# Kernel optimization log

Hardware: AMD Instinct MI355X
Metric: run time of the kernel (lower is better)

Reference implementation:

```python
import jax, jax.numpy as jnp
import numpy as np

IMG_H, IMG_W = 800.0, 1280.0
STRIDE = 16
SCALE = 1.0 / STRIDE
P, S = 14, 1              # pooler resolution, sampling ratio
NUM_CLASSES = 80
BBOX_W = (10.0, 10.0, 5.0, 5.0)
SCORE_TH, NMS_TH, MAX_DET, IOU_TH = 0.05, 0.5, 100, 0.5
SCALE_CLAMP = float(np.log(1000.0 / 16.0))


def _make_boxes(key, n_img, n_box):
    k1, k2, k3, k4 = jax.random.split(key, 4)
    x1 = jax.random.uniform(k1, (n_img, n_box)) * (IMG_W - 64.0)
    y1 = jax.random.uniform(k2, (n_img, n_box)) * (IMG_H - 64.0)
    w = jax.random.uniform(k3, (n_img, n_box)) * 300.0 + 16.0
    h = jax.random.uniform(k4, (n_img, n_box)) * 300.0 + 16.0
    x2 = jnp.minimum(x1 + w, IMG_W)
    y2 = jnp.minimum(y1 + h, IMG_H)
    return jnp.stack([x1, y1, x2, y2], axis=-1)


def setup_inputs() -> dict:
    key = jax.random.key(0)
    ks = jax.random.split(key, 6)
    features = jax.random.normal(ks[0], (2, 50, 80, 1024), dtype=jnp.float32)
    proposals = _make_boxes(ks[1], 2, 256)
    gt_boxes = _make_boxes(ks[2], 2, 64)
    gt_classes = jax.random.randint(ks[3], (2, 64), 0, NUM_CLASSES)
    W_cls = jax.random.normal(ks[4], (1024, NUM_CLASSES + 1), dtype=jnp.float32) * 0.01
    b_cls = jnp.zeros((NUM_CLASSES + 1,), jnp.float32)
    W_box = jax.random.normal(ks[5], (1024, 4), dtype=jnp.float32) * 0.01
    b_box = jnp.zeros((4,), jnp.float32)
    return {"features": features, "proposals": proposals, "gt_boxes": gt_boxes,
            "gt_classes": gt_classes, "W_cls": W_cls, "b_cls": b_cls,
            "W_box": W_box, "b_box": b_box}


def pairwise_iou(a, b):
    # a: [G,4], b: [R,4], boxes as (x1,y1,x2,y2) -> [G,R]
    area_a = (a[:, 2] - a[:, 0]) * (a[:, 3] - a[:, 1])
    area_b = (b[:, 2] - b[:, 0]) * (b[:, 3] - b[:, 1])
    lt = jnp.maximum(a[:, None, :2], b[None, :, :2])
    rb = jnp.minimum(a[:, None, 2:], b[None, :, 2:])
    wh = jnp.clip(rb - lt, 0.0)
    inter = wh[..., 0] * wh[..., 1]
    return inter / jnp.maximum(area_a[:, None] + area_b[None, :] - inter, 1e-9)


def roi_align_one(feat, boxes):
    # feat: [H,W,C], boxes: [R,4] in image coords -> pooled [R,P,P,C]
    H, W, C = feat.shape
    b = boxes * SCALE
    x1, y1, x2, y2 = b[:, 0], b[:, 1], b[:, 2], b[:, 3]
    off = (jnp.arange(S, dtype=feat.dtype) + 0.5) / S       # [S]
    grid = jnp.arange(P, dtype=feat.dtype)                   # [P]
    bh = ((y2 - y1) / P)[:, None, None]
    bw = ((x2 - x1) / P)[:, None, None]
    # aligned RoIAlign sample coords (half-pixel offset)
    gy = y1[:, None, None] + (grid[None, :, None] + off[None, None, :]) * bh - 0.5  # [R,P,S]
    gx = x1[:, None, None] + (grid[None, :, None] + off[None, None, :]) * bw - 0.5
    gy = jnp.clip(gy, 0.0, H - 1.0)
    gx = jnp.clip(gx, 0.0, W - 1.0)
    y0 = jnp.floor(gy); x0 = jnp.floor(gx)
    y0i = y0.astype(jnp.int32); x0i = x0.astype(jnp.int32)
    y1i = jnp.minimum(y0i + 1, H - 1); x1i = jnp.minimum(x0i + 1, W - 1)
    ly = gy - y0; lx = gx - x0

    def g(yi, xi):  # cross-product gather -> [R,P,S,P,S,C]
        return feat[yi[:, :, :, None, None], xi[:, None, None, :, :]]

    wy0 = (1.0 - ly)[:, :, :, None, None, None]; wy1 = ly[:, :, :, None, None, None]
    wx0 = (1.0 - lx)[:, None, None, :, :, None]; wx1 = lx[:, None, None, :, :, None]
    val = wy0 * (wx0 * g(y0i, x0i) + wx1 * g(y0i, x1i)) \
        + wy1 * (wx0 * g(y1i, x0i) + wx1 * g(y1i, x1i))
    return val.mean(axis=(2, 4))  # average sampling points per bin -> [R,P,P,C]


def decode_boxes(deltas, boxes):
    wx, wy, ww, wh = BBOX_W
    widths = boxes[..., 2] - boxes[..., 0]
    heights = boxes[..., 3] - boxes[..., 1]
    ctr_x = boxes[..., 0] + 0.5 * widths
    ctr_y = boxes[..., 1] + 0.5 * heights
    dx = deltas[..., 0] / wx
    dy = deltas[..., 1] / wy
    dw = jnp.minimum(deltas[..., 2] / ww, SCALE_CLAMP)
    dh = jnp.minimum(deltas[..., 3] / wh, SCALE_CLAMP)
    pcx = dx * widths + ctr_x
    pcy = dy * heights + ctr_y
    pw = jnp.exp(dw) * widths
    ph = jnp.exp(dh) * heights
    out = jnp.stack([pcx - 0.5 * pw, pcy - 0.5 * ph, pcx + 0.5 * pw, pcy + 0.5 * ph], axis=-1)
    lim = jnp.array([IMG_W, IMG_H, IMG_W, IMG_H], out.dtype)
    return jnp.clip(out, 0.0, lim)


def nms_keep(boxes, scores):
    # greedy class-agnostic NMS, fixed-size keep mask [R]
    R = scores.shape[0]
    order = jnp.argsort(-scores)
    sb = boxes[order]
    iou = pairwise_iou(sb, sb)
    idx = jnp.arange(R)

    def body(i, keep):
        suppressed = jnp.any((idx < i) & keep & (iou[:, i] > NMS_TH))
        return keep.at[i].set(jnp.logical_not(suppressed))

    keep_sorted = jax.lax.fori_loop(0, R, body, jnp.ones((R,), bool))
    return jnp.zeros((R,), bool).at[order].set(keep_sorted)


def reference(features, proposals, gt_boxes, gt_classes, W_cls, b_cls, W_box, b_box):
    N, R = proposals.shape[:2]
    # --- proposal <-> gt matching (training-side labeling) ---
    iou_m = jax.vmap(pairwise_iou)(gt_boxes, proposals)          # [N,G,R]
    matched_vals = iou_m.max(axis=1)
    matched_idxs = iou_m.argmax(axis=1)                          # [N,R]
    match_labels = (matched_vals >= IOU_TH).astype(jnp.int32)    # [N,R] fg=1/bg=0
    # --- RoIAlign pooling on the single C4 feature map ---
    pooled = jax.vmap(roi_align_one)(features, proposals)        # [N,R,P,P,C]
    feat_vec = pooled.mean(axis=(2, 3))                          # res5 surrogate global avg -> [N,R,C]
    # --- box predictor ---
    scores_all = jax.nn.softmax(feat_vec @ W_cls + b_cls, axis=-1)
    fg_scores = scores_all[..., :NUM_CLASSES].max(axis=-1)       # drop background column
    deltas = feat_vec @ W_box + b_box
    boxes = decode_boxes(deltas, proposals)                      # [N,R,4]
    # --- score threshold + NMS + top-k ---
    keep = jax.vmap(nms_keep)(boxes, fg_scores) & (fg_scores > SCORE_TH)
    masked = jnp.where(keep, fg_scores, -jnp.inf)
    rank = jnp.argsort(jnp.argsort(-masked, axis=-1), axis=-1)
    keep = keep & (rank < MAX_DET)
    det = jnp.concatenate([boxes, fg_scores[..., None], keep.astype(boxes.dtype)[..., None]], axis=-1)
    return det, matched_idxs, match_labels
```

## Files before the change

kernel.cpp:

```cpp
#include <hip/hip_runtime.h>
#include <math.h>

#define N_IMG 2
#define R_PROP 256
#define G_GT 64
#define C_CH 1024
#define FH 50
#define FW 80
#define P_POOL 14
#define NCLS 80
#define IMG_W_F 1280.0f
#define IMG_H_F 800.0f
#define SCALE_F 0.0625f
#define SCORE_TH_F 0.05f
#define NMS_TH_F 0.5f
#define IOU_TH_F 0.5f
#define MAX_DET_I 100
#define SCALE_CLAMP_F 4.135166556742356f

__global__ __launch_bounds__(512) void prep_kernel(
    const float* __restrict__ proposals,
    const float* __restrict__ gt_boxes,
    int* __restrict__ perm,
    float* __restrict__ out_idx,
    float* __restrict__ out_lbl) {
  const int t = threadIdx.x;
  const int n = t >> 8;
  __shared__ float cy[N_IMG * R_PROP];
  const float* pb = proposals + (size_t)t * 4;
  float bx1 = pb[0], by1 = pb[1], bx2 = pb[2], by2 = pb[3];
  cy[t] = by1 + by2;
  __syncthreads();

  {
    float my = cy[t];
    int rk = 0;
    const int base = n * R_PROP;
#pragma unroll 8
    for (int j = base; j < base + R_PROP; ++j) {
      float cj = cy[j];
      rk += (cj < my) || (cj == my && j < t);
    }
    perm[base + rk] = t & 255;
  }

  {
    float area_b = (bx2 - bx1) * (by2 - by1);
    float best = -1.0f;
    int bidx = 0;
    const float* gt = gt_boxes + (size_t)n * G_GT * 4;
#pragma unroll 4
    for (int g = 0; g < G_GT; ++g) {
      float gx1 = gt[g * 4 + 0], gy1 = gt[g * 4 + 1];
      float gx2 = gt[g * 4 + 2], gy2 = gt[g * 4 + 3];
      float area_a = (gx2 - gx1) * (gy2 - gy1);
      float ix1 = fmaxf(gx1, bx1), iy1 = fmaxf(gy1, by1);
      float ix2 = fminf(gx2, bx2), iy2 = fminf(gy2, by2);
      float iw = fmaxf(ix2 - ix1, 0.0f), ih = fmaxf(iy2 - iy1, 0.0f);
      float inter = iw * ih;
      float iou = inter / fmaxf(area_a + area_b - inter, 1e-9f);
      if (iou > best) { best = iou; bidx = g; }
    }
    out_idx[t] = (float)bidx;
    out_lbl[t] = (best >= IOU_TH_F) ? 1.0f : 0.0f;
  }
}

__global__ __launch_bounds__(1024) void roihead_kernel(
    const float* __restrict__ features,
    const float* __restrict__ proposals,
    const int* __restrict__ perm,
    const float* __restrict__ W_cls,
    const float* __restrict__ W_box,
    float* __restrict__ part) {
  const int b = blockIdx.x;
  const int xcd = b & 7;
  const int slot = b >> 3;
  const int n = xcd >> 2;
  const int band = xcd & 3;
  const int h = slot & 1;
  const int blk = n * R_PROP + perm[n * R_PROP + band * 64 + (slot >> 1)];

  const float* feat = features + (size_t)n * (FH * FW * C_CH) + h * (C_CH / 2);
  const int t = threadIdx.x;
  const int c4 = t & 127;
  const int g = t >> 7;

  __shared__ float s_Wy[FH];
  __shared__ float s_Wx[FW];
  __shared__ int s_b[4];
  __shared__ float4 s_red[7][128];
  __shared__ __align__(16) float sf[C_CH / 2];
  __shared__ float s_part[12][85];

  if (t < FH) s_Wy[t] = 0.0f;
  if (t >= 128 && t < 128 + FW) s_Wx[t - 128] = 0.0f;
  __syncthreads();

  if (t < 2 * P_POOL) {
    const float* pb = proposals + (size_t)blk * 4;
    bool isY = t < P_POOL;
    int i = isY ? t : t - P_POOL;
    float lo = isY ? pb[1] : pb[0];
    float hi = isY ? pb[3] : pb[2];
    float limit = isY ? (float)(FH - 1) : (float)(FW - 1);
    float b1 = lo * SCALE_F, b2 = hi * SCALE_F;
    float bs = (b2 - b1) * (1.0f / P_POOL);
    float gg = b1 + ((float)i + 0.5f) * bs - 0.5f;
    gg = fminf(fmaxf(gg, 0.0f), limit);
    float fl = floorf(gg);
    int i0 = (int)fl;
    int i1 = min(i0 + 1, (int)limit);
    float l = gg - fl;
    if (isY) {
      atomicAdd(&s_Wy[i0], 1.0f - l);
      atomicAdd(&s_Wy[i1], l);
      if (i == 0) s_b[0] = i0;
      if (i == P_POOL - 1) s_b[1] = i1;
    } else {
      atomicAdd(&s_Wx[i0], 1.0f - l);
      atomicAdd(&s_Wx[i1], l);
      if (i == 0) s_b[2] = i0;
      if (i == P_POOL - 1) s_b[3] = i1;
    }
  }
  __syncthreads();

  {
    const int ylo = s_b[0], yhi = s_b[1], xlo = s_b[2], xhi = s_b[3];
    float4 acc = make_float4(0.f, 0.f, 0.f, 0.f);
    for (int y = ylo + g; y <= yhi; y += 8) {
      float wy = s_Wy[y];
      const float4* row = (const float4*)(feat + (size_t)y * (FW * C_CH)) + c4;
#pragma unroll 8
      for (int x = xlo; x <= xhi; ++x) {
        float w = wy * s_Wx[x];
        float4 f = row[x * (C_CH / 4)];
        acc.x += w * f.x;
        acc.y += w * f.y;
        acc.z += w * f.z;
        acc.w += w * f.w;
      }
    }
    if (g > 0) s_red[g - 1][c4] = acc;
    __syncthreads();
    if (g == 0) {
      const float inv = 1.0f / (float)(P_POOL * P_POOL);
#pragma unroll
      for (int p = 0; p < 7; ++p) {
        float4 a = s_red[p][c4];
        acc.x += a.x; acc.y += a.y; acc.z += a.z; acc.w += a.w;
      }
      ((float4*)sf)[c4] =
          make_float4(acc.x * inv, acc.y * inv, acc.z * inv, acc.w * inv);
    }
    __syncthreads();
  }

  const int kq = t / 85;
  const int j = t - kq * 85;
  if (kq < 12) {
    float acc = 0.0f;
    const int kbase = h * (C_CH / 2);
    if (j < 81) {
      const float* __restrict__ w = W_cls + (size_t)kbase * 81 + j;
#pragma unroll 8
      for (int k = kq; k < C_CH / 2; k += 12) acc += sf[k] * w[k * 81];
    } else {
      const float* __restrict__ w = W_box + (size_t)kbase * 4 + (j - 81);
#pragma unroll 8
      for (int k = kq; k < C_CH / 2; k += 12) acc += sf[k] * w[k * 4];
    }
    s_part[kq][j] = acc;
  }
  __syncthreads();

  if (t < 85) {
    float acc = 0.0f;
#pragma unroll
    for (int p = 0; p < 12; ++p) acc += s_part[p][t];
    part[(size_t)blk * 170 + h * 85 + t] = acc;
  }
}

__global__ __launch_bounds__(128) void finalize_kernel(
    const float* __restrict__ part,
    const float* __restrict__ proposals,
    const float* __restrict__ b_cls,
    const float* __restrict__ b_box,
    float* __restrict__ boxes_dec,
    float* __restrict__ scores) {
  const int blk = blockIdx.x;
  const int t = threadIdx.x;
  __shared__ float sl[85];
  __shared__ float s_red[8];

  const float* pp = part + (size_t)blk * 170;
  if (t < 85) {
    float bias = (t < 81) ? b_cls[t] : b_box[t - 81];
    sl[t] = pp[t] + pp[85 + t] + bias;
  }
  __syncthreads();

  {
    float xm = (t < 81) ? sl[t] : -INFINITY;
    float xf = (t < NCLS) ? sl[t] : -INFINITY;
#pragma unroll
    for (int off = 32; off; off >>= 1) {
      xm = fmaxf(xm, __shfl_down(xm, off, 64));
      xf = fmaxf(xf, __shfl_down(xf, off, 64));
    }
    if ((t & 63) == 0) { s_red[t >> 6] = xm; s_red[2 + (t >> 6)] = xf; }
  }
  __syncthreads();
  const float m = fmaxf(s_red[0], s_red[1]);
  {
    float xs = (t < 81) ? expf(sl[t] - m) : 0.0f;
#pragma unroll
    for (int off = 32; off; off >>= 1) xs += __shfl_down(xs, off, 64);
    if ((t & 63) == 0) s_red[4 + (t >> 6)] = xs;
  }
  __syncthreads();

  if (t == 0) {
    float sum = s_red[4] + s_red[5];
    float fgm = fmaxf(s_red[2], s_red[3]);
    scores[blk] = expf(fgm - m) / sum;

    const float* pb = proposals + (size_t)blk * 4;
    float w = pb[2] - pb[0], h = pb[3] - pb[1];
    float cx = pb[0] + 0.5f * w, cy = pb[1] + 0.5f * h;
    float dx = sl[81] * 0.1f;
    float dy = sl[82] * 0.1f;
    float dw = fminf(sl[83] * 0.2f, SCALE_CLAMP_F);
    float dh = fminf(sl[84] * 0.2f, SCALE_CLAMP_F);
    float pcx = dx * w + cx, pcy = dy * h + cy;
    float pw = expf(dw) * w, ph = expf(dh) * h;
    float ox1 = fminf(fmaxf(pcx - 0.5f * pw, 0.0f), IMG_W_F);
    float oy1 = fminf(fmaxf(pcy - 0.5f * ph, 0.0f), IMG_H_F);
    float ox2 = fminf(fmaxf(pcx + 0.5f * pw, 0.0f), IMG_W_F);
    float oy2 = fminf(fmaxf(pcy + 0.5f * ph, 0.0f), IMG_H_F);
    float* bd = boxes_dec + (size_t)blk * 4;
    bd[0] = ox1; bd[1] = oy1; bd[2] = ox2; bd[3] = oy2;
  }
}

__global__ __launch_bounds__(1024) void nms_kernel(
    const float* __restrict__ boxes_dec,
    const float* __restrict__ scores,
    float* __restrict__ det) {
  const int n = blockIdx.x;
  const int u = threadIdx.x;
  const int i = u & 255;
  const int q = u >> 8;
  const int j40 = q * 16;

  __shared__ __align__(16) float ss[R_PROP];
  __shared__ float4 sbs[R_PROP];
  __shared__ int s_part[4 * R_PROP];
  __shared__ int s_rank[R_PROP];
  __shared__ __align__(16) unsigned long long s_mask[R_PROP * 4];
  __shared__ unsigned long long s_keep[4];
  __shared__ __align__(16) float sm[R_PROP];

  float4 myb;
  float mys;
  if (q == 0) {
    myb = ((const float4*)boxes_dec)[n * R_PROP + i];
    mys = scores[n * R_PROP + i];
    ss[i] = mys;
  }
  __syncthreads();

  {
    float s = ss[i];
    int cnt = 0;
#pragma unroll
    for (int j4 = j40; j4 < j40 + 16; ++j4) {
      float4 v = ((const float4*)ss)[j4];
      int jb = j4 * 4;
      cnt += (v.x > s) || (v.x == s && jb + 0 < i);
      cnt += (v.y > s) || (v.y == s && jb + 1 < i);
      cnt += (v.z > s) || (v.z == s && jb + 2 < i);
      cnt += (v.w > s) || (v.w == s && jb + 3 < i);
    }
    s_part[q * R_PROP + i] = cnt;
  }
  __syncthreads();
  if (q == 0) {
    int rk = s_part[i] + s_part[R_PROP + i] + s_part[2 * R_PROP + i] +
             s_part[3 * R_PROP + i];
    s_rank[i] = rk;
    sbs[rk] = myb;
  }
  __syncthreads();

  {
    float4 bi = sbs[i];
    float area_i = (bi.z - bi.x) * (bi.w - bi.y);
    unsigned long long m = 0;
    const int j0 = q * 64;
#pragma unroll 8
    for (int jj = 0; jj < 64; ++jj) {
      float4 bj = sbs[j0 + jj];
      float area_j = (bj.z - bj.x) * (bj.w - bj.y);
      float ix1 = fmaxf(bi.x, bj.x), iy1 = fmaxf(bi.y, bj.y);
      float ix2 = fminf(bi.z, bj.z), iy2 = fminf(bi.w, bj.w);
      float iw = fmaxf(ix2 - ix1, 0.0f), ih = fmaxf(iy2 - iy1, 0.0f);
      float inter = iw * ih;
      float iou = inter / fmaxf(area_i + area_j - inter, 1e-9f);
      m |= (iou > NMS_TH_F) ? (1ull << jj) : 0ull;
    }
    s_mask[i * 4 + q] = m;
  }
  __syncthreads();

  if (u == 0) {
    unsigned long long K0 = ~0ull, K1 = ~0ull, K2 = ~0ull, K3 = ~0ull;
#pragma unroll 16
    for (int b = 1; b < 64; ++b) {
      unsigned long long m0 = s_mask[(size_t)b * 4 + 0];
      unsigned long long sup = m0 & K0 & ((1ull << b) - 1ull);
      K0 = sup ? (K0 & ~(1ull << b)) : K0;
    }
#pragma unroll 16
    for (int b = 0; b < 64; ++b) {
      const unsigned long long* mi = &s_mask[(size_t)(64 + b) * 4];
      unsigned long long m0 = mi[0], m1 = mi[1];
      unsigned long long sup = (m0 & K0) | (m1 & K1 & ((1ull << b) - 1ull));
      K1 = sup ? (K1 & ~(1ull << b)) : K1;
    }
#pragma unroll 16
    for (int b = 0; b < 64; ++b) {
      const unsigned long long* mi = &s_mask[(size_t)(128 + b) * 4];
      unsigned long long m0 = mi[0], m1 = mi[1], m2 = mi[2];
      unsigned long long sup =
          (m0 & K0) | (m1 & K1) | (m2 & K2 & ((1ull << b) - 1ull));
      K2 = sup ? (K2 & ~(1ull << b)) : K2;
    }
#pragma unroll 16
    for (int b = 0; b < 64; ++b) {
      const unsigned long long* mi = &s_mask[(size_t)(192 + b) * 4];
      unsigned long long m0 = mi[0], m1 = mi[1], m2 = mi[2], m3 = mi[3];
      unsigned long long sup = (m0 & K0) | (m1 & K1) | (m2 & K2) |
                               (m3 & K3 & ((1ull << b) - 1ull));
      K3 = sup ? (K3 & ~(1ull << b)) : K3;
    }
    s_keep[0] = K0; s_keep[1] = K1; s_keep[2] = K2; s_keep[3] = K3;
  }
  __syncthreads();

  bool kept = false;
  if (q == 0) {
    int rk = s_rank[i];
    kept = ((s_keep[rk >> 6] >> (rk & 63)) & 1ull) && (mys > SCORE_TH_F);
    sm[i] = kept ? mys : -INFINITY;
  }
  __syncthreads();

  {
    float mym = sm[i];
    int cnt = 0;
#pragma unroll
    for (int j4 = j40; j4 < j40 + 16; ++j4) {
      float4 v = ((const float4*)sm)[j4];
      int jb = j4 * 4;
      cnt += (v.x > mym) || (v.x == mym && jb + 0 < i);
      cnt += (v.y > mym) || (v.y == mym && jb + 1 < i);
      cnt += (v.z > mym) || (v.z == mym && jb + 2 < i);
      cnt += (v.w > mym) || (v.w == mym && jb + 3 < i);
    }
    s_part[q * R_PROP + i] = cnt;
  }
  __syncthreads();

  if (q == 0) {
    int rk2 = s_part[i] + s_part[R_PROP + i] + s_part[2 * R_PROP + i] +
              s_part[3 * R_PROP + i];
    kept = kept && (rk2 < MAX_DET_I);
    float* dr = det + ((size_t)n * R_PROP + i) * 6;
    dr[0] = myb.x; dr[1] = myb.y; dr[2] = myb.z; dr[3] = myb.w;
    dr[4] = mys;
    dr[5] = kept ? 1.0f : 0.0f;
  }
}

extern "C" void kernel_launch(void* const* d_in, const int* in_sizes, int n_in,
                              void* d_out, int out_size, void* d_ws, size_t ws_size,
                              hipStream_t stream) {
  const float* features  = (const float*)d_in[0];
  const float* proposals = (const float*)d_in[1];
  const float* gt_boxes  = (const float*)d_in[2];
  const float* W_cls = (const float*)d_in[4];
  const float* b_cls = (const float*)d_in[5];
  const float* W_box = (const float*)d_in[6];
  const float* b_box = (const float*)d_in[7];

  float* out = (float*)d_out;
  float* out_det = out;
  float* out_idx = out + N_IMG * R_PROP * 6;
  float* out_lbl = out_idx + N_IMG * R_PROP;

  float* part      = (float*)d_ws;
  float* boxes_dec = part + (size_t)N_IMG * R_PROP * 170;
  float* scores    = boxes_dec + (size_t)N_IMG * R_PROP * 4;
  int*   perm      = (int*)(scores + N_IMG * R_PROP);

  prep_kernel<<<1, 512, 0, stream>>>(proposals, gt_boxes, perm, out_idx, out_lbl);
  roihead_kernel<<<2 * N_IMG * R_PROP, 1024, 0, stream>>>(
      features, proposals, perm, W_cls, W_box, part);
  finalize_kernel<<<N_IMG * R_PROP, 128, 0, stream>>>(
      part, proposals, b_cls, b_box, boxes_dec, scores);
  nms_kernel<<<N_IMG, 1024, 0, stream>>>(boxes_dec, scores, out_det);
}
```

Before: 165.9 us.

## Fuse finalize into roihead and process full channel range per block

Each proposal is now handled by a single block covering all 1024 channels, replacing the previous split of channel halves across two blocks. This allows the softmax, score, and box-decode finalize step to run inside the same kernel, which removes the partial-logit workspace round trip and one kernel launch. In exchange, the block count halves to 512 and each thread group strides over rows with 4 groups instead of 8. Each thread also does twice the matvec work over K, which may lower parallelism and latency hiding in the bandwidth-bound pooling phase.

```diff
diff --git a/kernel.cpp b/kernel.cpp
--- a/kernel.cpp
+++ b/kernel.cpp
@@ -72,26 +72,30 @@
     const int* __restrict__ perm,
     const float* __restrict__ W_cls,
     const float* __restrict__ W_box,
-    float* __restrict__ part) {
+    const float* __restrict__ b_cls,
+    const float* __restrict__ b_box,
+    float* __restrict__ boxes_dec,
+    float* __restrict__ scores) {
   const int b = blockIdx.x;
   const int xcd = b & 7;
   const int slot = b >> 3;
   const int n = xcd >> 2;
   const int band = xcd & 3;
-  const int h = slot & 1;
-  const int blk = n * R_PROP + perm[n * R_PROP + band * 64 + (slot >> 1)];
-
-  const float* feat = features + (size_t)n * (FH * FW * C_CH) + h * (C_CH / 2);
+  const int blk = n * R_PROP + perm[n * R_PROP + band * 64 + slot];
+
+  const float* feat = features + (size_t)n * (FH * FW * C_CH);
   const int t = threadIdx.x;
-  const int c4 = t & 127;
-  const int g = t >> 7;
+  const int c4 = t & 255;
+  const int g = t >> 8;
 
   __shared__ float s_Wy[FH];
   __shared__ float s_Wx[FW];
   __shared__ int s_b[4];
-  __shared__ float4 s_red[7][128];
-  __shared__ __align__(16) float sf[C_CH / 2];
+  __shared__ float4 s_red[3][256];
+  __shared__ __align__(16) float sf[C_CH];
   __shared__ float s_part[12][85];
+  __shared__ float sl[85];
+  __shared__ float s_red2[8];
 
   if (t < FH) s_Wy[t] = 0.0f;
   if (t >= 128 && t < 128 + FW) s_Wx[t - 128] = 0.0f;
@@ -129,7 +133,7 @@
   {
     const int ylo = s_b[0], yhi = s_b[1], xlo = s_b[2], xhi = s_b[3];
     float4 acc = make_float4(0.f, 0.f, 0.f, 0.f);
-    for (int y = ylo + g; y <= yhi; y += 8) {
+    for (int y = ylo + g; y <= yhi; y += 4) {
       float wy = s_Wy[y];
       const float4* row = (const float4*)(feat + (size_t)y * (FW * C_CH)) + c4;
 #pragma unroll 8
@@ -147,7 +151,7 @@
     if (g == 0) {
       const float inv = 1.0f / (float)(P_POOL * P_POOL);
 #pragma unroll
-      for (int p = 0; p < 7; ++p) {
+      for (int p = 0; p < 3; ++p) {
         float4 a = s_red[p][c4];
         acc.x += a.x; acc.y += a.y; acc.z += a.z; acc.w += a.w;
       }
@@ -157,52 +161,35 @@
     __syncthreads();
   }
 
-  const int kq = t / 85;
-  const int j = t - kq * 85;
-  if (kq < 12) {
-    float acc = 0.0f;
-    const int kbase = h * (C_CH / 2);
-    if (j < 81) {
-      const float* __restrict__ w = W_cls + (size_t)kbase * 81 + j;
+  {
+    const int kq = t / 85;
+    const int j = t - kq * 85;
+    if (kq < 12) {
+      float acc = 0.0f;
+      if (j < 81) {
+        const float* __restrict__ w = W_cls + j;
 #pragma unroll 8
-      for (int k = kq; k < C_CH / 2; k += 12) acc += sf[k] * w[k * 81];
-    } else {
-      const float* __restrict__ w = W_box + (size_t)kbase * 4 + (j - 81);
+        for (int k = kq; k < C_CH; k += 12) acc += sf[k] * w[k * 81];
+      } else {
+        const float* __restrict__ w = W_box + (j - 81);
 #pragma unroll 8
-      for (int k = kq; k < C_CH / 2; k += 12) acc += sf[k] * w[k * 4];
-    }
-    s_part[kq][j] = acc;
-  }
-  __syncthreads();
-
-  if (t < 85) {
-    float acc = 0.0f;
-#pragma unroll
-    for (int p = 0; p < 12; ++p) acc += s_part[p][t];
-    part[(size_t)blk * 170 + h * 85 + t] = acc;
-  }
-}
-
-__global__ __launch_bounds__(128) void finalize_kernel(
-    const float* __restrict__ part,
-    const float* __restrict__ proposals,
-    const float* __restrict__ b_cls,
-    const float* __restrict__ b_box,
-    float* __restrict__ boxes_dec,
-    float* __restrict__ scores) {
-  const int blk = blockIdx.x;
-  const int t = threadIdx.x;
-  __shared__ float sl[85];
-  __shared__ float s_red[8];
-
-  const float* pp = part + (size_t)blk * 170;
+        for (int k = kq; k < C_CH; k += 12) acc += sf[k] * w[k * 4];
+      }
+      s_part[kq][j] = acc;
+    }
+  }
+  __syncthreads();
+
   if (t < 85) {
     float bias = (t < 81) ? b_cls[t] : b_box[t - 81];
-    sl[t] = pp[t] + pp[85 + t] + bias;
-  }
-  __syncthreads();
-
-  {
+    float acc = bias;
+#pragma unroll
+    for (int p = 0; p < 12; ++p) acc += s_part[p][t];
+    sl[t] = acc;
+  }
+  __syncthreads();
+
+  if (t < 128) {
     float xm = (t < 81) ? sl[t] : -INFINITY;
     float xf = (t < NCLS) ? sl[t] : -INFINITY;
 #pragma unroll
@@ -210,31 +197,32 @@
       xm = fmaxf(xm, __shfl_down(xm, off, 64));
       xf = fmaxf(xf, __shfl_down(xf, off, 64));
     }
-    if ((t & 63) == 0) { s_red[t >> 6] = xm; s_red[2 + (t >> 6)] = xf; }
-  }
-  __syncthreads();
-  const float m = fmaxf(s_red[0], s_red[1]);
-  {
+    if ((t & 63) == 0) { s_red2[t >> 6] = xm; s_red2[2 + (t >> 6)] = xf; }
+  }
+  __syncthreads();
+  if (t < 128) {
+    const float m = fmaxf(s_red2[0], s_red2[1]);
     float xs = (t < 81) ? expf(sl[t] - m) : 0.0f;
 #pragma unroll
     for (int off = 32; off; off >>= 1) xs += __shfl_down(xs, off, 64);
-    if ((t & 63) == 0) s_red[4 + (t >> 6)] = xs;
+    if ((t & 63) == 0) s_red2[4 + (t >> 6)] = xs;
   }
   __syncthreads();
 
   if (t == 0) {
-    float sum = s_red[4] + s_red[5];
-    float fgm = fmaxf(s_red[2], s_red[3]);
+    const float m = fmaxf(s_red2[0], s_red2[1]);
+    float sum = s_red2[4] + s_red2[5];
+    float fgm = fmaxf(s_red2[2], s_red2[3]);
     scores[blk] = expf(fgm - m) / sum;
 
     const float* pb = proposals + (size_t)blk * 4;
     float w = pb[2] - pb[0], h = pb[3] - pb[1];
-    float cx = pb[0] + 0.5f * w, cy = pb[1] + 0.5f * h;
+    float cx = pb[0] + 0.5f * w, cyc = pb[1] + 0.5f * h;
     float dx = sl[81] * 0.1f;
     float dy = sl[82] * 0.1f;
     float dw = fminf(sl[83] * 0.2f, SCALE_CLAMP_F);
     float dh = fminf(sl[84] * 0.2f, SCALE_CLAMP_F);
-    float pcx = dx * w + cx, pcy = dy * h + cy;
+    float pcx = dx * w + cx, pcy = dy * h + cyc;
     float pw = expf(dw) * w, ph = expf(dh) * h;
     float ox1 = fminf(fmaxf(pcx - 0.5f * pw, 0.0f), IMG_W_F);
     float oy1 = fminf(fmaxf(pcy - 0.5f * ph, 0.0f), IMG_H_F);
@@ -401,15 +389,12 @@
   float* out_idx = out + N_IMG * R_PROP * 6;
   float* out_lbl = out_idx + N_IMG * R_PROP;
 
-  float* part      = (float*)d_ws;
-  float* boxes_dec = part + (size_t)N_IMG * R_PROP * 170;
+  float* boxes_dec = (float*)d_ws;
   float* scores    = boxes_dec + (size_t)N_IMG * R_PROP * 4;
   int*   perm      = (int*)(scores + N_IMG * R_PROP);
 
   prep_kernel<<<1, 512, 0, stream>>>(proposals, gt_boxes, perm, out_idx, out_lbl);
-  roihead_kernel<<<2 * N_IMG * R_PROP, 1024, 0, stream>>>(
-      features, proposals, perm, W_cls, W_box, part);
-  finalize_kernel<<<N_IMG * R_PROP, 128, 0, stream>>>(
-      part, proposals, b_cls, b_box, boxes_dec, scores);
+  roihead_kernel<<<N_IMG * R_PROP, 1024, 0, stream>>>(
+      features, proposals, perm, W_cls, W_box, b_cls, b_box, boxes_dec, scores);
   nms_kernel<<<N_IMG, 1024, 0, stream>>>(boxes_dec, scores, out_det);
 }
```

New measurement: 167.5 us. About the same (+0.9%).

## Use persistent workers with cost-sorted dynamic task queue and quarter-channel split

Applied to the files above, without the earlier changes.

The prep kernel now estimates each proposal's pooling cost from its footprint on the feature grid and sorts all proposals by descending cost. The RoI head becomes a persistent kernel of 1024 blocks with 512 threads each, pulling tasks from a global atomic counter. Each task is one proposal and one quarter of the channels, and finalize sums four partials instead of two. This aims to balance the uneven per-RoI work (longest first), but gives up the previous per-XCD image/band placement that may have helped L2 locality, and adds an atomic per task.

```diff
diff --git a/kernel.cpp b/kernel.cpp
--- a/kernel.cpp
+++ b/kernel.cpp
@@ -18,30 +18,51 @@
 #define MAX_DET_I 100
 #define SCALE_CLAMP_F 4.135166556742356f
 
+#define NQ 4
+#define NTASK (N_IMG * R_PROP * NQ)
+#define QCH (C_CH / NQ)
+
 __global__ __launch_bounds__(512) void prep_kernel(
     const float* __restrict__ proposals,
     const float* __restrict__ gt_boxes,
-    int* __restrict__ perm,
+    int* __restrict__ sq,
+    int* __restrict__ counter,
     float* __restrict__ out_idx,
     float* __restrict__ out_lbl) {
   const int t = threadIdx.x;
   const int n = t >> 8;
-  __shared__ float cy[N_IMG * R_PROP];
+  __shared__ int s_cost[N_IMG * R_PROP];
+
   const float* pb = proposals + (size_t)t * 4;
   float bx1 = pb[0], by1 = pb[1], bx2 = pb[2], by2 = pb[3];
-  cy[t] = by1 + by2;
-  __syncthreads();
-
-  {
-    float my = cy[t];
+  if (t == 0) counter[0] = 0;
+
+  {
+    float b1y = by1 * SCALE_F, b2y = by2 * SCALE_F;
+    float bsy = (b2y - b1y) * (1.0f / P_POOL);
+    float gy0  = fminf(fmaxf(b1y + 0.5f  * bsy - 0.5f, 0.0f), (float)(FH - 1));
+    float gy13 = fminf(fmaxf(b1y + 13.5f * bsy - 0.5f, 0.0f), (float)(FH - 1));
+    int ylo = (int)floorf(gy0);
+    int yhi = min((int)floorf(gy13) + 1, FH - 1);
+    float b1x = bx1 * SCALE_F, b2x = bx2 * SCALE_F;
+    float bsx = (b2x - b1x) * (1.0f / P_POOL);
+    float gx0  = fminf(fmaxf(b1x + 0.5f  * bsx - 0.5f, 0.0f), (float)(FW - 1));
+    float gx13 = fminf(fmaxf(b1x + 13.5f * bsx - 0.5f, 0.0f), (float)(FW - 1));
+    int xlo = (int)floorf(gx0);
+    int xhi = min((int)floorf(gx13) + 1, FW - 1);
+    s_cost[t] = (yhi - ylo + 1) * (xhi - xlo + 1);
+  }
+  __syncthreads();
+
+  {
+    int myc = s_cost[t];
     int rk = 0;
-    const int base = n * R_PROP;
 #pragma unroll 8
-    for (int j = base; j < base + R_PROP; ++j) {
-      float cj = cy[j];
-      rk += (cj < my) || (cj == my && j < t);
-    }
-    perm[base + rk] = t & 255;
+    for (int j = 0; j < N_IMG * R_PROP; ++j) {
+      int cj = s_cost[j];
+      rk += (cj > myc) || (cj == myc && j < t);
+    }
+    sq[rk] = t;
   }
 
   {
@@ -66,120 +87,125 @@
   }
 }
 
-__global__ __launch_bounds__(1024) void roihead_kernel(
+__global__ __launch_bounds__(512) void roihead_kernel(
     const float* __restrict__ features,
     const float* __restrict__ proposals,
-    const int* __restrict__ perm,
+    const int* __restrict__ sq,
     const float* __restrict__ W_cls,
     const float* __restrict__ W_box,
+    int* __restrict__ counter,
     float* __restrict__ part) {
-  const int b = blockIdx.x;
-  const int xcd = b & 7;
-  const int slot = b >> 3;
-  const int n = xcd >> 2;
-  const int band = xcd & 3;
-  const int h = slot & 1;
-  const int blk = n * R_PROP + perm[n * R_PROP + band * 64 + (slot >> 1)];
-
-  const float* feat = features + (size_t)n * (FH * FW * C_CH) + h * (C_CH / 2);
   const int t = threadIdx.x;
-  const int c4 = t & 127;
-  const int g = t >> 7;
+  const int c4 = t & 63;
+  const int g = t >> 6;
 
   __shared__ float s_Wy[FH];
   __shared__ float s_Wx[FW];
   __shared__ int s_b[4];
-  __shared__ float4 s_red[7][128];
-  __shared__ __align__(16) float sf[C_CH / 2];
-  __shared__ float s_part[12][85];
-
-  if (t < FH) s_Wy[t] = 0.0f;
-  if (t >= 128 && t < 128 + FW) s_Wx[t - 128] = 0.0f;
-  __syncthreads();
-
-  if (t < 2 * P_POOL) {
-    const float* pb = proposals + (size_t)blk * 4;
-    bool isY = t < P_POOL;
-    int i = isY ? t : t - P_POOL;
-    float lo = isY ? pb[1] : pb[0];
-    float hi = isY ? pb[3] : pb[2];
-    float limit = isY ? (float)(FH - 1) : (float)(FW - 1);
-    float b1 = lo * SCALE_F, b2 = hi * SCALE_F;
-    float bs = (b2 - b1) * (1.0f / P_POOL);
-    float gg = b1 + ((float)i + 0.5f) * bs - 0.5f;
-    gg = fminf(fmaxf(gg, 0.0f), limit);
-    float fl = floorf(gg);
-    int i0 = (int)fl;
-    int i1 = min(i0 + 1, (int)limit);
-    float l = gg - fl;
-    if (isY) {
-      atomicAdd(&s_Wy[i0], 1.0f - l);
-      atomicAdd(&s_Wy[i1], l);
-      if (i == 0) s_b[0] = i0;
-      if (i == P_POOL - 1) s_b[1] = i1;
-    } else {
-      atomicAdd(&s_Wx[i0], 1.0f - l);
-      atomicAdd(&s_Wx[i1], l);
-      if (i == 0) s_b[2] = i0;
-      if (i == P_POOL - 1) s_b[3] = i1;
-    }
-  }
-  __syncthreads();
-
-  {
-    const int ylo = s_b[0], yhi = s_b[1], xlo = s_b[2], xhi = s_b[3];
-    float4 acc = make_float4(0.f, 0.f, 0.f, 0.f);
-    for (int y = ylo + g; y <= yhi; y += 8) {
-      float wy = s_Wy[y];
-      const float4* row = (const float4*)(feat + (size_t)y * (FW * C_CH)) + c4;
+  __shared__ float4 s_red[7][64];
+  __shared__ __align__(16) float sf[QCH];
+  __shared__ float s_part[6][85];
+  __shared__ int s_tid;
+
+  for (;;) {
+    __syncthreads();
+    if (t < FH) s_Wy[t] = 0.0f;
+    if (t >= 128 && t < 128 + FW) s_Wx[t - 128] = 0.0f;
+    if (t == 0) s_tid = atomicAdd(counter, 1);
+    __syncthreads();
+    const int tid = s_tid;
+    if (tid >= NTASK) break;
+
+    const int p = sq[tid >> 2];
+    const int q = tid & 3;
+    const int qbase = q * QCH;
+    const float* feat = features + (size_t)(p >> 8) * (FH * FW * C_CH) + qbase;
+
+    if (t < 2 * P_POOL) {
+      const float* pb = proposals + (size_t)p * 4;
+      bool isY = t < P_POOL;
+      int i = isY ? t : t - P_POOL;
+      float lo = isY ? pb[1] : pb[0];
+      float hi = isY ? pb[3] : pb[2];
+      float limit = isY ? (float)(FH - 1) : (float)(FW - 1);
+      float b1 = lo * SCALE_F, b2 = hi * SCALE_F;
+      float bs = (b2 - b1) * (1.0f / P_POOL);
+      float gg = b1 + ((float)i + 0.5f) * bs - 0.5f;
+      gg = fminf(fmaxf(gg, 0.0f), limit);
+      float fl = floorf(gg);
+      int i0 = (int)fl;
+      int i1 = min(i0 + 1, (int)limit);
+      float l = gg - fl;
+      if (isY) {
+        atomicAdd(&s_Wy[i0], 1.0f - l);
+        atomicAdd(&s_Wy[i1], l);
+        if (i == 0) s_b[0] = i0;
+        if (i == P_POOL - 1) s_b[1] = i1;
+      } else {
+        atomicAdd(&s_Wx[i0], 1.0f - l);
+        atomicAdd(&s_Wx[i1], l);
+        if (i == 0) s_b[2] = i0;
+        if (i == P_POOL - 1) s_b[3] = i1;
+      }
+    }
+    __syncthreads();
+
+    {
+      const int ylo = s_b[0], yhi = s_b[1], xlo = s_b[2], xhi = s_b[3];
+      float4 acc = make_float4(0.f, 0.f, 0.f, 0.f);
+      for (int y = ylo + g; y <= yhi; y += 8) {
+        float wy = s_Wy[y];
+        const float4* row = (const float4*)(feat + (size_t)y * (FW * C_CH)) + c4;
 #pragma unroll 8
-      for (int x = xlo; x <= xhi; ++x) {
-        float w = wy * s_Wx[x];
-        float4 f = row[x * (C_CH / 4)];
-        acc.x += w * f.x;
-        acc.y += w * f.y;
-        acc.z += w * f.z;
-        acc.w += w * f.w;
+        for (int x = xlo; x <= xhi; ++x) {
+          float w = wy * s_Wx[x];
+          float4 f = row[x * (C_CH / 4)];
+          acc.x += w * f.x;
+          acc.y += w * f.y;
+          acc.z += w * f.z;
+          acc.w += w * f.w;
+        }
       }
-    }
-    if (g > 0) s_red[g - 1][c4] = acc;
+      if (g > 0) s_red[g - 1][c4] = acc;
+      __syncthreads();
+      if (g == 0) {
+        const float inv = 1.0f / (float)(P_POOL * P_POOL);
+#pragma unroll
+        for (int r = 0; r < 7; ++r) {
+          float4 a = s_red[r][c4];
+          acc.x += a.x; acc.y += a.y; acc.z += a.z; acc.w += a.w;
+        }
+        ((float4*)sf)[c4] =
+            make_float4(acc.x * inv, acc.y * inv, acc.z * inv, acc.w * inv);
+      }
+      __syncthreads();
+    }
+
+    {
+      const int kq = t / 85;
+      const int j = t - kq * 85;
+      if (kq < 6) {
+        float acc = 0.0f;
+        if (j < 81) {
+          const float* __restrict__ w = W_cls + (size_t)qbase * 81 + j;
+#pragma unroll 8
+          for (int k = kq; k < QCH; k += 6) acc += sf[k] * w[k * 81];
+        } else {
+          const float* __restrict__ w = W_box + (size_t)qbase * 4 + (j - 81);
+#pragma unroll 8
+          for (int k = kq; k < QCH; k += 6) acc += sf[k] * w[k * 4];
+        }
+        s_part[kq][j] = acc;
+      }
+    }
     __syncthreads();
-    if (g == 0) {
-      const float inv = 1.0f / (float)(P_POOL * P_POOL);
-#pragma unroll
-      for (int p = 0; p < 7; ++p) {
-        float4 a = s_red[p][c4];
-        acc.x += a.x; acc.y += a.y; acc.z += a.z; acc.w += a.w;
-      }
-      ((float4*)sf)[c4] =
-          make_float4(acc.x * inv, acc.y * inv, acc.z * inv, acc.w * inv);
-    }
-    __syncthreads();
-  }
-
-  const int kq = t / 85;
-  const int j = t - kq * 85;
-  if (kq < 12) {
-    float acc = 0.0f;
-    const int kbase = h * (C_CH / 2);
-    if (j < 81) {
-      const float* __restrict__ w = W_cls + (size_t)kbase * 81 + j;
-#pragma unroll 8
-      for (int k = kq; k < C_CH / 2; k += 12) acc += sf[k] * w[k * 81];
-    } else {
-      const float* __restrict__ w = W_box + (size_t)kbase * 4 + (j - 81);
-#pragma unroll 8
-      for (int k = kq; k < C_CH / 2; k += 12) acc += sf[k] * w[k * 4];
-    }
-    s_part[kq][j] = acc;
-  }
-  __syncthreads();
-
-  if (t < 85) {
-    float acc = 0.0f;
-#pragma unroll
-    for (int p = 0; p < 12; ++p) acc += s_part[p][t];
-    part[(size_t)blk * 170 + h * 85 + t] = acc;
+
+    if (t < 85) {
+      float acc = 0.0f;
+#pragma unroll
+      for (int r = 0; r < 6; ++r) acc += s_part[r][t];
+      part[((size_t)p * NQ + q) * 85 + t] = acc;
+    }
   }
 }
 
@@ -195,10 +221,10 @@
   __shared__ float sl[85];
   __shared__ float s_red[8];
 
-  const float* pp = part + (size_t)blk * 170;
+  const float* pp = part + (size_t)blk * (NQ * 85);
   if (t < 85) {
     float bias = (t < 81) ? b_cls[t] : b_box[t - 81];
-    sl[t] = pp[t] + pp[85 + t] + bias;
+    sl[t] = pp[t] + pp[85 + t] + pp[170 + t] + pp[255 + t] + bias;
   }
   __syncthreads();
 
@@ -401,14 +427,16 @@
   float* out_idx = out + N_IMG * R_PROP * 6;
   float* out_lbl = out_idx + N_IMG * R_PROP;
 
-  float* part      = (float*)d_ws;
-  float* boxes_dec = part + (size_t)N_IMG * R_PROP * 170;
+  int*   counter   = (int*)d_ws;
+  int*   sq        = counter + 16;
+  float* part      = (float*)(sq + 512);
+  float* boxes_dec = part + (size_t)N_IMG * R_PROP * NQ * 85;
   float* scores    = boxes_dec + (size_t)N_IMG * R_PROP * 4;
-  int*   perm      = (int*)(scores + N_IMG * R_PROP);
-
-  prep_kernel<<<1, 512, 0, stream>>>(proposals, gt_boxes, perm, out_idx, out_lbl);
-  roihead_kernel<<<2 * N_IMG * R_PROP, 1024, 0, stream>>>(
-      features, proposals, perm, W_cls, W_box, part);
+
+  prep_kernel<<<1, 512, 0, stream>>>(proposals, gt_boxes, sq, counter,
+                                     out_idx, out_lbl);
+  roihead_kernel<<<1024, 512, 0, stream>>>(features, proposals, sq, W_cls,
+                                           W_box, counter, part);
   finalize_kernel<<<N_IMG * R_PROP, 128, 0, stream>>>(
       part, proposals, b_cls, b_box, boxes_dec, scores);
   nms_kernel<<<N_IMG, 1024, 0, stream>>>(boxes_dec, scores, out_det);
```

After: 199.4 us. 1.2x slower.

## Split RoI pooling into four channel quarters with 256-thread blocks

Applied to the files above, without the earlier changes.

The RoI head kernel now splits each proposal's 1024 channels into four quarters instead of two halves. Each quarter runs in a 256-thread block with 4 row groups instead of 1024 threads with 8, which doubles the grid and shrinks shared memory and reduction work per block. Finalize sums four partial logit vectors, and the workspace layout is reordered so perm comes first. The intent is better occupancy and load balance across CUs. In exchange, each block has less row parallelism and the partial writes and bilinear-weight setup grow.

```diff
diff --git a/kernel.cpp b/kernel.cpp
--- a/kernel.cpp
+++ b/kernel.cpp
@@ -18,6 +18,9 @@
 #define MAX_DET_I 100
 #define SCALE_CLAMP_F 4.135166556742356f
 
+#define NQ 4
+#define QCH (C_CH / NQ)
+
 __global__ __launch_bounds__(512) void prep_kernel(
     const float* __restrict__ proposals,
     const float* __restrict__ gt_boxes,
@@ -66,7 +69,7 @@
   }
 }
 
-__global__ __launch_bounds__(1024) void roihead_kernel(
+__global__ __launch_bounds__(256) void roihead_kernel(
     const float* __restrict__ features,
     const float* __restrict__ proposals,
     const int* __restrict__ perm,
@@ -78,27 +81,28 @@
   const int slot = b >> 3;
   const int n = xcd >> 2;
   const int band = xcd & 3;
-  const int h = slot & 1;
-  const int blk = n * R_PROP + perm[n * R_PROP + band * 64 + (slot >> 1)];
-
-  const float* feat = features + (size_t)n * (FH * FW * C_CH) + h * (C_CH / 2);
+  const int q = slot & 3;
+  const int p = n * R_PROP + perm[n * R_PROP + band * 64 + (slot >> 2)];
+  const int qbase = q * QCH;
+
+  const float* feat = features + (size_t)n * (FH * FW * C_CH) + qbase;
   const int t = threadIdx.x;
-  const int c4 = t & 127;
-  const int g = t >> 7;
+  const int c4 = t & 63;
+  const int g = t >> 6;
 
   __shared__ float s_Wy[FH];
   __shared__ float s_Wx[FW];
   __shared__ int s_b[4];
-  __shared__ float4 s_red[7][128];
-  __shared__ __align__(16) float sf[C_CH / 2];
-  __shared__ float s_part[12][85];
+  __shared__ float4 s_red[3][64];
+  __shared__ __align__(16) float sf[QCH];
+  __shared__ float s_part[3][85];
 
   if (t < FH) s_Wy[t] = 0.0f;
   if (t >= 128 && t < 128 + FW) s_Wx[t - 128] = 0.0f;
   __syncthreads();
 
   if (t < 2 * P_POOL) {
-    const float* pb = proposals + (size_t)blk * 4;
+    const float* pb = proposals + (size_t)p * 4;
     bool isY = t < P_POOL;
     int i = isY ? t : t - P_POOL;
     float lo = isY ? pb[1] : pb[0];
@@ -129,7 +133,7 @@
   {
     const int ylo = s_b[0], yhi = s_b[1], xlo = s_b[2], xhi = s_b[3];
     float4 acc = make_float4(0.f, 0.f, 0.f, 0.f);
-    for (int y = ylo + g; y <= yhi; y += 8) {
+    for (int y = ylo + g; y <= yhi; y += 4) {
       float wy = s_Wy[y];
       const float4* row = (const float4*)(feat + (size_t)y * (FW * C_CH)) + c4;
 #pragma unroll 8
@@ -147,8 +151,8 @@
     if (g == 0) {
       const float inv = 1.0f / (float)(P_POOL * P_POOL);
 #pragma unroll
-      for (int p = 0; p < 7; ++p) {
-        float4 a = s_red[p][c4];
+      for (int r = 0; r < 3; ++r) {
+        float4 a = s_red[r][c4];
         acc.x += a.x; acc.y += a.y; acc.z += a.z; acc.w += a.w;
       }
       ((float4*)sf)[c4] =
@@ -157,29 +161,28 @@
     __syncthreads();
   }
 
-  const int kq = t / 85;
-  const int j = t - kq * 85;
-  if (kq < 12) {
-    float acc = 0.0f;
-    const int kbase = h * (C_CH / 2);
-    if (j < 81) {
-      const float* __restrict__ w = W_cls + (size_t)kbase * 81 + j;
+  {
+    const int kq = t / 85;
+    const int j = t - kq * 85;
+    if (kq < 3) {
+      float acc = 0.0f;
+      if (j < 81) {
+        const float* __restrict__ w = W_cls + (size_t)qbase * 81 + j;
 #pragma unroll 8
-      for (int k = kq; k < C_CH / 2; k += 12) acc += sf[k] * w[k * 81];
-    } else {
-      const float* __restrict__ w = W_box + (size_t)kbase * 4 + (j - 81);
+        for (int k = kq; k < QCH; k += 3) acc += sf[k] * w[k * 81];
+      } else {
+        const float* __restrict__ w = W_box + (size_t)qbase * 4 + (j - 81);
 #pragma unroll 8
-      for (int k = kq; k < C_CH / 2; k += 12) acc += sf[k] * w[k * 4];
-    }
-    s_part[kq][j] = acc;
+        for (int k = kq; k < QCH; k += 3) acc += sf[k] * w[k * 4];
+      }
+      s_part[kq][j] = acc;
+    }
   }
   __syncthreads();
 
   if (t < 85) {
-    float acc = 0.0f;
-#pragma unroll
-    for (int p = 0; p < 12; ++p) acc += s_part[p][t];
-    part[(size_t)blk * 170 + h * 85 + t] = acc;
+    float acc = s_part[0][t] + s_part[1][t] + s_part[2][t];
+    part[((size_t)p * NQ + q) * 85 + t] = acc;
   }
 }
 
@@ -195,10 +198,10 @@
   __shared__ float sl[85];
   __shared__ float s_red[8];
 
-  const float* pp = part + (size_t)blk * 170;
+  const float* pp = part + (size_t)blk * (NQ * 85);
   if (t < 85) {
     float bias = (t < 81) ? b_cls[t] : b_box[t - 81];
-    sl[t] = pp[t] + pp[85 + t] + bias;
+    sl[t] = pp[t] + pp[85 + t] + pp[170 + t] + pp[255 + t] + bias;
   }
   __syncthreads();
 
@@ -401,13 +404,14 @@
   float* out_idx = out + N_IMG * R_PROP * 6;
   float* out_lbl = out_idx + N_IMG * R_PROP;
 
-  float* part      = (float*)d_ws;
-  float* boxes_dec = part + (size_t)N_IMG * R_PROP * 170;
+  int*   perm      = (int*)d_ws;
+  float* part      = (float*)(perm + 512);
+  float* boxes_dec = part + (size_t)N_IMG * R_PROP * NQ * 85;
   float* scores    = boxes_dec + (size_t)N_IMG * R_PROP * 4;
-  int*   perm      = (int*)(scores + N_IMG * R_PROP);
-
-  prep_kernel<<<1, 512, 0, stream>>>(proposals, gt_boxes, perm, out_idx, out_lbl);
-  roihead_kernel<<<2 * N_IMG * R_PROP, 1024, 0, stream>>>(
+
+  prep_kernel<<<1, 512, 0, stream>>>(proposals, gt_boxes, perm, out_idx,
+                                     out_lbl);
+  roihead_kernel<<<N_IMG * R_PROP * NQ, 256, 0, stream>>>(
       features, proposals, perm, W_cls, W_box, part);
   finalize_kernel<<<N_IMG * R_PROP, 128, 0, stream>>>(
       part, proposals, b_cls, b_box, boxes_dec, scores);
```

New measurement: 163.8 us (median of 2 runs). No clear change (-1.3%).
